# Optimization experiments

Measured on AMD Instinct MI355X. Metric: run time of the kernel, lower is better.

## Reference

```python
import jax, jax.numpy as jnp
import numpy as np

BETA = 0.25


def setup_inputs() -> dict:
    key = jax.random.key(0)
    k1, k2, k3, k4 = jax.random.split(key, 4)
    n_emb, emb_dim, in_ch = 16384, 256, 1024
    feats = jax.random.normal(k1, (8, in_ch, 32, 32), dtype=jnp.float32)
    conv_w = jax.random.normal(k2, (emb_dim, in_ch), dtype=jnp.float32) * (1.0 / np.sqrt(in_ch))
    conv_b = jax.random.normal(k3, (emb_dim,), dtype=jnp.float32) * 0.01
    # torch init: uniform(-1/n_emb, 1/n_emb)
    codebook = jax.random.uniform(k4, (n_emb, emb_dim), dtype=jnp.float32,
                                  minval=-1.0 / n_emb, maxval=1.0 / n_emb)
    return {"feats": feats, "conv_w": conv_w, "conv_b": conv_b, "codebook": codebook}


def reference(feats, conv_w, conv_b, codebook):
    sg = jax.lax.stop_gradient
    # 1x1 conv == channel GEMM: [B,C,H,W] -> [B,E,H,W]
    z = jnp.einsum('bchw,ec->behw', feats, conv_w) + conv_b[None, :, None, None]
    z = jnp.transpose(z, (0, 2, 3, 1))            # [B,H,W,E]
    B, H, W, E = z.shape
    zf = z.reshape(-1, E)                          # [N,E]
    # pairwise squared distances: ||z||^2 + ||e||^2 - 2 z.e^T
    d = (jnp.sum(zf * zf, axis=1, keepdims=True)
         + jnp.sum(codebook * codebook, axis=1)
         - 2.0 * zf @ codebook.T)                  # [N,n_emb]
    idx = jnp.argmin(d, axis=1)                    # [N]
    # one-hot matmul in original == direct gather (same math)
    z_q = codebook[idx].reshape(B, H, W, E)
    loss = jnp.mean((sg(z_q) - z) ** 2) + BETA * jnp.mean((z_q - sg(z)) ** 2)
    z_q = z + sg(z_q - z)                          # straight-through
    z_q = jnp.transpose(z_q, (0, 3, 1, 2))         # [B,E,H,W]
    return (z_q, loss)
```

## Files before the change

kernel.cpp:

```cpp
#include <hip/hip_runtime.h>
#include <hip/hip_bf16.h>
#include <stdint.h>


typedef float f32x4 __attribute__((ext_vector_type(4)));
typedef float f32x16 __attribute__((ext_vector_type(16)));
typedef short s16x8 __attribute__((ext_vector_type(8)));

__device__ __forceinline__ void gl2lds16(const void* g, void* l) {
  __builtin_amdgcn_global_load_lds(
      (const __attribute__((address_space(1))) void*)g,
      (__attribute__((address_space(3))) void*)l, 16, 0, 0);
}

__device__ __forceinline__ unsigned short f2bf(float f) {
  unsigned u = __float_as_uint(f);
  u = u + 0x7FFFu + ((u >> 16) & 1u);
  return (unsigned short)(u >> 16);
}
__device__ __forceinline__ float bf2f(unsigned short u) {
  return __uint_as_float(((unsigned)u) << 16);
}

__device__ __forceinline__ ushort4 cvt4(float4 v) {
  ushort4 o;
  o.x = f2bf(v.x); o.y = f2bf(v.y); o.z = f2bf(v.z); o.w = f2bf(v.w);
  return o;
}

__global__ void k_prep(const float* __restrict__ cbk, const float* __restrict__ Wsrc,
                       const float* __restrict__ feats,
                       unsigned short* __restrict__ cbs, unsigned short* __restrict__ W2,
                       unsigned short* __restrict__ At, float* __restrict__ lossw) {
  __shared__ float tile[64][65];
  int blk = blockIdx.x, t = threadIdx.x;
  if (blk == 0 && t < 2) ((int*)lossw)[t] = 0;
  if (blk < 256) {
    int jt = blk;
    #pragma unroll
    for (int lp = 0; lp < 8; ++lp) {
      int fl = lp * 256 + t;
      int ks = fl >> 7, fr = (fl >> 6) & 1, lane = fl & 63;
      int j = jt * 64 + fr * 32 + (lane & 31);
      int k = ks * 16 + (lane >> 5) * 8;
      const float* src = cbk + (size_t)j * 256 + k;
      float4 v0 = *(const float4*)(src);
      float4 v1 = *(const float4*)(src + 4);
      unsigned short* dst = cbs + ((size_t)jt * 2048 + fl) * 8;
      *(ushort4*)(dst) = cvt4(v0);
      *(ushort4*)(dst + 4) = cvt4(v1);
    }
  } else if (blk < 384) {
    size_t base = (size_t)(blk - 256) * 2048 + t * 8;
    float4 v0 = *(const float4*)(Wsrc + base);
    float4 v1 = *(const float4*)(Wsrc + base + 4);
    *(ushort4*)(W2 + base) = cvt4(v0);
    *(ushort4*)(W2 + base + 4) = cvt4(v1);
  } else {
    int id = blk - 384;
    int b = id >> 8, c0 = ((id >> 4) & 15) * 64, s0 = (id & 15) * 64;
    int tc = t >> 4, ts = (t & 15) * 4;
    #pragma unroll
    for (int k = 0; k < 4; ++k) {
      float4 v = *(const float4*)(feats + ((size_t)b * 1024 + c0 + tc + k * 16) * 1024 + s0 + ts);
      tile[tc + k * 16][ts] = v.x;
      tile[tc + k * 16][ts + 1] = v.y;
      tile[tc + k * 16][ts + 2] = v.z;
      tile[tc + k * 16][ts + 3] = v.w;
    }
    __syncthreads();
    #pragma unroll
    for (int k = 0; k < 4; ++k) {
      int sr = tc + k * 16;
      float4 v;
      v.x = tile[ts][sr]; v.y = tile[ts + 1][sr];
      v.z = tile[ts + 2][sr]; v.w = tile[ts + 3][sr];
      *(ushort4*)(At + (size_t)(b * 1024 + s0 + sr) * 1024 + c0 + ts) = cvt4(v);
    }
  }
}

__global__ __launch_bounds__(256, 2)
void k_gemm1(const unsigned short* __restrict__ At, const unsigned short* __restrict__ Bw,
             const float* __restrict__ bias, unsigned short* __restrict__ zb) {
  __shared__ __align__(16) uint8_t lds[1024 * 16];
  uint8_t* ldsA = lds;
  uint8_t* ldsB = lds + 512 * 16;
  const int t = threadIdx.x, w = t >> 6, l = t & 63;
  const int wy = w >> 1, wx = w & 1, l15 = l & 15, q = l >> 4;
  const int ib = blockIdx.y * 64, eb = blockIdx.x * 64;
  f32x4 acc[2][2] = {};
  for (int kt = 0; kt < 16; ++kt) {
    int c0 = kt * 64;
    __syncthreads();
    #pragma unroll
    for (int r = 0; r < 2; ++r) {
      int P = t + 256 * r;
      gl2lds16(At + (size_t)(ib + (P & 63)) * 1024 + c0 + (P >> 6) * 8, ldsA + P * 16);
    }
    #pragma unroll
    for (int r = 0; r < 2; ++r) {
      int P = t + 256 * r;
      gl2lds16(Bw + (size_t)(eb + (P & 63)) * 1024 + c0 + (P >> 6) * 8, ldsB + P * 16);
    }
    __syncthreads();
    #pragma unroll
    for (int s = 0; s < 2; ++s) {
      s16x8 a[2], b[2];
      #pragma unroll
      for (int fr = 0; fr < 2; ++fr)
        a[fr] = *(const s16x8*)(ldsA + ((s * 4 + q) * 64 + wy * 32 + fr * 16 + l15) * 16);
      #pragma unroll
      for (int fc = 0; fc < 2; ++fc)
        b[fc] = *(const s16x8*)(ldsB + ((s * 4 + q) * 64 + wx * 32 + fc * 16 + l15) * 16);
      #pragma unroll
      for (int fr = 0; fr < 2; ++fr)
        #pragma unroll
        for (int fc = 0; fc < 2; ++fc)
          acc[fr][fc] = __builtin_amdgcn_mfma_f32_16x16x32_bf16(a[fr], b[fc], acc[fr][fc], 0, 0, 0);
    }
  }
  #pragma unroll
  for (int fc = 0; fc < 2; ++fc) {
    int e = eb + wx * 32 + fc * 16 + l15;
    float bv = bias[e];
    #pragma unroll
    for (int fr = 0; fr < 2; ++fr)
      #pragma unroll
      for (int r = 0; r < 4; ++r) {
        int i = ib + wy * 32 + fr * 16 + q * 4 + r;
        zb[(size_t)i * 256 + e] = f2bf(acc[fr][fc][r] + bv);
      }
  }
}

__global__ __launch_bounds__(256, 3)
void k_gemm2(const unsigned short* __restrict__ cbs, const unsigned short* __restrict__ zb,
             int* __restrict__ cand) {
  __shared__ __align__(16) uint8_t ldsB[2048 * 16];
  __shared__ int csh[4][64];
  const int t = threadIdx.x, w = t >> 6, l = t & 63;
  const int l31 = l & 31, h = l >> 5;
  const int ib = blockIdx.y * 64;
  #pragma unroll
  for (int r = 0; r < 8; ++r) {
    int P = t + 256 * r;
    gl2lds16(zb + (size_t)(ib + (P & 63)) * 256 + (P >> 6) * 8, ldsB + P * 16);
  }
  int rbest[2];
  rbest[0] = rbest[1] = (int)0x80000000;
  __syncthreads();
  #pragma unroll 1
  for (int js = 0; js < 2; ++js) {
    const int jtile = blockIdx.x * 8 + js * 4 + w;
    const int jw = jtile * 64;
    const uint8_t* abase = (const uint8_t*)cbs + (size_t)jtile * 32768 + l * 16;
    f32x16 acc[2][2] = {};
    #pragma unroll 4
    for (int ks = 0; ks < 16; ++ks) {
      s16x8 a[2], b[2];
      #pragma unroll
      for (int fr = 0; fr < 2; ++fr)
        a[fr] = *(const s16x8*)(abase + (ks * 2 + fr) * 1024);
      #pragma unroll
      for (int fc = 0; fc < 2; ++fc)
        b[fc] = *(const s16x8*)(ldsB + ((ks * 2 + h) * 64 + fc * 32 + l31) * 16);
      #pragma unroll
      for (int fr = 0; fr < 2; ++fr)
        #pragma unroll
        for (int fc = 0; fc < 2; ++fc)
          acc[fr][fc] = __builtin_amdgcn_mfma_f32_32x32x16_bf16(a[fr], b[fc], acc[fr][fc], 0, 0, 0);
    }
    const int encb = 16383 - (jw + 4 * h);
    #pragma unroll
    for (int fc = 0; fc < 2; ++fc) {
      int bb = rbest[fc];
      #pragma unroll
      for (int fr = 0; fr < 2; ++fr) {
        const int e1 = encb - fr * 32;
        #pragma unroll
        for (int rg = 0; rg < 16; ++rg) {
          int e = e1 - ((rg & 3) + 8 * (rg >> 2));
          int m = __float_as_int(3.0f + acc[fr][fc][rg]);
          int p = (int)(((unsigned)m << 14) + (unsigned)e);
          bb = p > bb ? p : bb;
        }
      }
      rbest[fc] = bb;
    }
  }
  #pragma unroll
  for (int fc = 0; fc < 2; ++fc) {
    int bb = max(rbest[fc], __shfl_xor(rbest[fc], 32, 64));
    if (l < 32) csh[w][fc * 32 + l31] = bb;
  }
  __syncthreads();
  if (t < 64) {
    int m0 = max(max(csh[0][t], csh[1][t]), max(csh[2][t], csh[3][t]));
    cand[(size_t)blockIdx.x * 8192 + ib + t] = m0;
  }
}

__global__ void k_final(const unsigned short* __restrict__ zb, const int* __restrict__ cand,
                        const float* __restrict__ cbk, float* __restrict__ lossw,
                        float* __restrict__ out) {
  __shared__ int lidx[64];
  __shared__ float ps[4];
  int blk = blockIdx.x, t = threadIdx.x;
  int b = blk >> 4, s0 = (blk & 15) * 64;
  int row = t >> 2, c = t & 3;
  int gi = b * 1024 + s0 + row;
  const unsigned short* zrow = zb + (size_t)gi * 256 + c * 64;
  float ss = 0.0f;
  #pragma unroll
  for (int k = 0; k < 64; k += 4) {
    ushort4 v = *(const ushort4*)(zrow + k);
    float a0 = bf2f(v.x), a1 = bf2f(v.y), a2 = bf2f(v.z), a3 = bf2f(v.w);
    ss += a0 * a0 + a1 * a1 + a2 * a2 + a3 * a3;
  }
  int best = (int)0x80000000;
  #pragma unroll
  for (int k = 0; k < 8; ++k) {
    int v = cand[(size_t)(c + 4 * k) * 8192 + gi];
    best = v > best ? v : best;
  }
  best = max(best, __shfl_xor(best, 1, 64));
  best = max(best, __shfl_xor(best, 2, 64));
  ss += __shfl_xor(ss, 1, 64);
  ss += __shfl_xor(ss, 2, 64);
  float dist = 0.0f;
  if (c == 0) {
    lidx[row] = 16383 - (best & 0x3FFF);
    dist = ss - (float)(best >> 14) * (1.0f / 1048576.0f);
  }
  float v = dist;
  #pragma unroll
  for (int m = 32; m; m >>= 1) v += __shfl_down(v, m, 64);
  if ((t & 63) == 0) ps[t >> 6] = v;
  __syncthreads();
  if (t == 0) {
    float part = ps[0] + ps[1] + ps[2] + ps[3];
    atomicAdd(lossw, part);
    __threadfence();
    int cnt = atomicAdd((int*)lossw + 1, 1);
    if (cnt == 127) {
      __threadfence();
      float total = atomicAdd(lossw, 0.0f);
      out[2097152] = 1.25f * total * (1.0f / 2097152.0f);
    }
  }
  int sl = t & 63, e0 = t >> 6;
  size_t ob = (size_t)b * 262144 + s0 + sl;
  size_t crow = (size_t)lidx[sl] * 256;
  for (int e = e0; e < 256; e += 4)
    out[ob + (size_t)e * 1024] = cbk[crow + e];
}

extern "C" void kernel_launch(void* const* d_in, const int* in_sizes, int n_in,
                              void* d_out, int out_size, void* d_ws, size_t ws_size,
                              hipStream_t stream) {
  const float* feats  = (const float*)d_in[0];
  const float* conv_w = (const float*)d_in[1];
  const float* conv_b = (const float*)d_in[2];
  const float* cbk    = (const float*)d_in[3];
  float* out = (float*)d_out;
  char* ws = (char*)d_ws;
  unsigned short* featsT = (unsigned short*)(ws);
  unsigned short* W2     = (unsigned short*)(ws + 16777216);
  unsigned short* cbs    = (unsigned short*)(ws + 17301504);
  unsigned short* zb     = (unsigned short*)(ws + 25690112);
  int*            cand   = (int*)(ws + 29884416);
  float*          lossw  = (float*)(ws + 30932992);

  k_prep<<<2432, 256, 0, stream>>>(cbk, conv_w, feats, cbs, W2, featsT, lossw);
  k_gemm1<<<dim3(4, 128), 256, 0, stream>>>(featsT, W2, conv_b, zb);
  k_gemm2<<<dim3(32, 128), 256, 0, stream>>>(cbs, zb, cand);
  k_final<<<128, 256, 0, stream>>>(zb, cand, cbk, lossw, out);
}
```

Baseline: 201.1 us.

## Double gemm1 K-tile, raise gemm2 occupancy, split final into argmin and gather kernels

Result: faster. 196.6 us (-2.3%).

```diff
diff --git a/kernel.cpp b/kernel.cpp
--- a/kernel.cpp
+++ b/kernel.cpp
@@ -83,29 +83,29 @@
 __global__ __launch_bounds__(256, 2)
 void k_gemm1(const unsigned short* __restrict__ At, const unsigned short* __restrict__ Bw,
              const float* __restrict__ bias, unsigned short* __restrict__ zb) {
-  __shared__ __align__(16) uint8_t lds[1024 * 16];
+  __shared__ __align__(16) uint8_t lds[2048 * 16];
   uint8_t* ldsA = lds;
-  uint8_t* ldsB = lds + 512 * 16;
+  uint8_t* ldsB = lds + 1024 * 16;
   const int t = threadIdx.x, w = t >> 6, l = t & 63;
   const int wy = w >> 1, wx = w & 1, l15 = l & 15, q = l >> 4;
   const int ib = blockIdx.y * 64, eb = blockIdx.x * 64;
   f32x4 acc[2][2] = {};
-  for (int kt = 0; kt < 16; ++kt) {
-    int c0 = kt * 64;
+  for (int kt = 0; kt < 8; ++kt) {
+    int c0 = kt * 128;
     __syncthreads();
     #pragma unroll
-    for (int r = 0; r < 2; ++r) {
+    for (int r = 0; r < 4; ++r) {
       int P = t + 256 * r;
       gl2lds16(At + (size_t)(ib + (P & 63)) * 1024 + c0 + (P >> 6) * 8, ldsA + P * 16);
     }
     #pragma unroll
-    for (int r = 0; r < 2; ++r) {
+    for (int r = 0; r < 4; ++r) {
       int P = t + 256 * r;
       gl2lds16(Bw + (size_t)(eb + (P & 63)) * 1024 + c0 + (P >> 6) * 8, ldsB + P * 16);
     }
     __syncthreads();
     #pragma unroll
-    for (int s = 0; s < 2; ++s) {
+    for (int s = 0; s < 4; ++s) {
       s16x8 a[2], b[2];
       #pragma unroll
       for (int fr = 0; fr < 2; ++fr)
@@ -134,7 +134,7 @@
   }
 }
 
-__global__ __launch_bounds__(256, 3)
+__global__ __launch_bounds__(256, 4)
 void k_gemm2(const unsigned short* __restrict__ cbs, const unsigned short* __restrict__ zb,
              int* __restrict__ cand) {
   __shared__ __align__(16) uint8_t ldsB[2048 * 16];
@@ -201,15 +201,13 @@
   }
 }
 
-__global__ void k_final(const unsigned short* __restrict__ zb, const int* __restrict__ cand,
-                        const float* __restrict__ cbk, float* __restrict__ lossw,
-                        float* __restrict__ out) {
-  __shared__ int lidx[64];
+__global__ void k_argmin(const unsigned short* __restrict__ zb, const int* __restrict__ cand,
+                         int* __restrict__ idx, float* __restrict__ lossw,
+                         float* __restrict__ out) {
   __shared__ float ps[4];
   int blk = blockIdx.x, t = threadIdx.x;
-  int b = blk >> 4, s0 = (blk & 15) * 64;
   int row = t >> 2, c = t & 3;
-  int gi = b * 1024 + s0 + row;
+  int gi = blk * 64 + row;
   const unsigned short* zrow = zb + (size_t)gi * 256 + c * 64;
   float ss = 0.0f;
   #pragma unroll
@@ -230,7 +228,7 @@
   ss += __shfl_xor(ss, 2, 64);
   float dist = 0.0f;
   if (c == 0) {
-    lidx[row] = 16383 - (best & 0x3FFF);
+    idx[gi] = 16383 - (best & 0x3FFF);
     dist = ss - (float)(best >> 14) * (1.0f / 1048576.0f);
   }
   float v = dist;
@@ -249,11 +247,33 @@
       out[2097152] = 1.25f * total * (1.0f / 2097152.0f);
     }
   }
-  int sl = t & 63, e0 = t >> 6;
+}
+
+__global__ void k_gather(const float* __restrict__ cbk, const int* __restrict__ idx,
+                         float* __restrict__ out) {
+  __shared__ float tile[32][257];
+  __shared__ int lidx[32];
+  int blk = blockIdx.x, t = threadIdx.x;
+  int b = blk >> 5, s0 = (blk & 31) * 32;
+  if (t < 32) lidx[t] = idx[b * 1024 + s0 + t];
+  __syncthreads();
+  int w = t >> 6, l = t & 63;
+  #pragma unroll
+  for (int rr = 0; rr < 8; ++rr) {
+    int r = w * 8 + rr;
+    const float* src = cbk + (size_t)lidx[r] * 256;
+    #pragma unroll
+    for (int k = 0; k < 4; ++k)
+      tile[r][l + 64 * k] = src[l + 64 * k];
+  }
+  __syncthreads();
+  int sl = t & 31, eg = t >> 5;
   size_t ob = (size_t)b * 262144 + s0 + sl;
-  size_t crow = (size_t)lidx[sl] * 256;
-  for (int e = e0; e < 256; e += 4)
-    out[ob + (size_t)e * 1024] = cbk[crow + e];
+  #pragma unroll
+  for (int k = 0; k < 32; ++k) {
+    int e = eg + 8 * k;
+    out[ob + (size_t)e * 1024] = tile[sl][e];
+  }
 }
 
 extern "C" void kernel_launch(void* const* d_in, const int* in_sizes, int n_in,
@@ -270,10 +290,12 @@
   unsigned short* cbs    = (unsigned short*)(ws + 17301504);
   unsigned short* zb     = (unsigned short*)(ws + 25690112);
   int*            cand   = (int*)(ws + 29884416);
-  float*          lossw  = (float*)(ws + 30932992);
+  int*            idx    = (int*)(ws + 30932992);
+  float*          lossw  = (float*)(ws + 30965760);
 
   k_prep<<<2432, 256, 0, stream>>>(cbk, conv_w, feats, cbs, W2, featsT, lossw);
   k_gemm1<<<dim3(4, 128), 256, 0, stream>>>(featsT, W2, conv_b, zb);
   k_gemm2<<<dim3(32, 128), 256, 0, stream>>>(cbs, zb, cand);
-  k_final<<<128, 256, 0, stream>>>(zb, cand, cbk, lossw, out);
-}
+  k_argmin<<<128, 256, 0, stream>>>(zb, cand, idx, lossw, out);
+  k_gather<<<256, 256, 0, stream>>>(cbk, idx, out);
+}
```
